# Performance work log

Hardware: AMD Instinct MI355X
Metric: run time of the kernel (lower is better)

## Reference

```python
import jax, jax.numpy as jnp
import numpy as np

N = 50000   # nodes
E = 800000  # edges (avg degree 16)
G = 64      # graphs in batch
DIMS = [96, 96, 96]  # gcn_layers_dim
RELU_LAYERS = [0, 1]


def setup_inputs() -> dict:
    key = jax.random.key(0)
    ks = jax.random.split(key, 32)
    inp = {
        "x": jax.random.normal(ks[0], (N, DIMS[0]), dtype=jnp.float32),
        "edge_index": jax.random.randint(ks[1], (2, E), 0, N, dtype=jnp.int64),
        "edge_weight": jax.random.uniform(ks[2], (E,), dtype=jnp.float32),
        "batch": jnp.sort(jax.random.randint(ks[3], (N,), 0, G, dtype=jnp.int64)),
        "edge_index_neighbor": jax.random.randint(ks[4], (2, E), 0, N, dtype=jnp.int64),
        "edge_weight_neighbor": jax.random.uniform(ks[5], (E,), dtype=jnp.float32),
        "batch_neighbor": jnp.sort(jax.random.randint(ks[6], (N,), 0, G, dtype=jnp.int64)),
    }
    ki = 7
    for l in range(len(DIMS) - 1):
        din, dout = DIMS[l], DIMS[l + 1]
        s = 1.0 / np.sqrt(din)
        inp[f"W{l}_o"] = jax.random.uniform(ks[ki + 0], (din, dout), minval=-s, maxval=s, dtype=jnp.float32)
        inp[f"b{l}_o"] = jnp.zeros((dout,), dtype=jnp.float32)
        inp[f"W{l}_n"] = jax.random.uniform(ks[ki + 1], (din, dout), minval=-s, maxval=s, dtype=jnp.float32)
        inp[f"b{l}_n"] = jnp.zeros((dout,), dtype=jnp.float32)
        sf = 1.0 / np.sqrt(2 * dout)
        inp[f"W{l}_f"] = jax.random.uniform(ks[ki + 2], (2 * dout, dout), minval=-sf, maxval=sf, dtype=jnp.float32)
        inp[f"b{l}_f"] = jax.random.uniform(ks[ki + 3], (dout,), minval=-sf, maxval=sf, dtype=jnp.float32)
        ki += 4
    return inp


def gcn_conv(x, W, b, edge_index, edge_weight, n):
    # PyG GCNConv: add self loops (weight 1), symmetric normalization, scatter-add.
    src, dst = edge_index[0], edge_index[1]
    deg = jax.ops.segment_sum(edge_weight, dst, num_segments=n) + 1.0  # +1 self loop
    dinv = jnp.where(deg > 0, jax.lax.rsqrt(deg), 0.0)  # [N]
    xw = x @ W  # [N, dout]
    norm = dinv[src] * edge_weight * dinv[dst]  # [E]
    out = jax.ops.segment_sum(norm[:, None] * xw[src], dst, num_segments=n)
    out = out + (dinv * dinv)[:, None] * xw  # self-loop contribution
    return out + b


def mean_pool(h, batch, g):
    s = jax.ops.segment_sum(h, batch, num_segments=g)
    c = jax.ops.segment_sum(jnp.ones((h.shape[0],), dtype=h.dtype), batch, num_segments=g)
    return s / jnp.maximum(c, 1.0)[:, None]


def reference(x, edge_index, edge_weight, batch, edge_index_neighbor,
              edge_weight_neighbor, batch_neighbor,
              W0_o, b0_o, W0_n, b0_n, W0_f, b0_f,
              W1_o, b1_o, W1_n, b1_n, W1_f, b1_f):
    params = [(W0_o, b0_o, W0_n, b0_n, W0_f, b0_f),
              (W1_o, b1_o, W1_n, b1_n, W1_f, b1_f)]
    n = x.shape[0]
    out = x
    embeddings = []
    for l, (Wo, bo, Wn, bn, Wf, bf) in enumerate(params):
        h_o = gcn_conv(out, Wo, bo, edge_index, edge_weight, n)
        h_n = gcn_conv(out, Wn, bn, edge_index_neighbor, edge_weight_neighbor, n)
        out = jnp.concatenate([h_o, h_n], axis=-1) @ Wf + bf
        if l in RELU_LAYERS:
            out = jax.nn.relu(out)
        embeddings.append(mean_pool(out, batch, G))
    return tuple(embeddings)
```

## Files before the change

### kernel.cpp

```cpp
#include <hip/hip_runtime.h>
#include <hip/hip_bf16.h>
#include <hip/hip_fp16.h>

#define DIM 96
#define EBLK 256
typedef unsigned int u32;
typedef unsigned long long u64;
typedef __attribute__((ext_vector_type(8))) _Float16 half8;
typedef __attribute__((ext_vector_type(4))) float f32x4;

__device__ __forceinline__ unsigned short f2h(float f) {
    union { unsigned short s; _Float16 h; } v; v.h = (_Float16)f; return v.s;
}
__device__ __forceinline__ u32 pkh(float lo, float hi) {
    return (u32)f2h(lo) | ((u32)f2h(hi) << 16);
}
__device__ __forceinline__ float hl(u32 u) {
    union { unsigned short s; _Float16 h; } v; v.s = (unsigned short)u; return (float)v.h;
}
__device__ __forceinline__ float hh(u32 u) {
    union { unsigned short s; _Float16 h; } v; v.s = (unsigned short)(u >> 16); return (float)v.h;
}

struct __align__(4) U3 { u32 a, b, c; };

__global__ __launch_bounds__(256) void k_cast0(
    const float* __restrict__ x, u32* __restrict__ Xh,
    const int* __restrict__ batch, int* __restrict__ gs, int* __restrict__ ge,
    float* __restrict__ outp, u32* __restrict__ cursor,
    int n, int total8, int osz)
{
    int i = blockIdx.x * 256 + threadIdx.x;
    if (i < total8) {
        const float4* xv = (const float4*)x;
        float4 a = xv[i * 2], b = xv[i * 2 + 1];
        uint4 o;
        o.x = pkh(a.x, a.y); o.y = pkh(a.z, a.w);
        o.z = pkh(b.x, b.y); o.w = pkh(b.z, b.w);
        ((uint4*)Xh)[i] = o;
    }
    if (i < n) {
        int b = batch[i];
        if (i == 0 || batch[i - 1] != b) gs[b] = i;
        if (i == n - 1 || batch[i + 1] != b) ge[b] = i + 1;
    }
    if (i < osz) outp[i] = 0.f;
    if (i == 0) { cursor[0] = 0; cursor[1] = 0; }
}

__global__ __launch_bounds__(256) void k_hist(
    const int* __restrict__ ei, const int* __restrict__ ein,
    u32* __restrict__ cntmat, int E, int n, int NB, int epb,
    const float* __restrict__ W0o, const float* __restrict__ W0n, const float* __restrict__ W0f,
    const float* __restrict__ b0o, const float* __restrict__ b0n, const float* __restrict__ b0f,
    const float* __restrict__ W1o, const float* __restrict__ W1n, const float* __restrict__ W1f,
    const float* __restrict__ b1o, const float* __restrict__ b1n, const float* __restrict__ b1f,
    unsigned short* __restrict__ Wt, float* __restrict__ bc,
    const int* __restrict__ gs, const int* __restrict__ ge, float* __restrict__ rinv)
{
    int set = blockIdx.y, tid = threadIdx.x;
    if (blockIdx.x >= EBLK) {
        if (blockIdx.y == 0 && blockIdx.x == EBLK && tid < 64) {
            int c = ge[tid] - gs[tid];
            if (c < 1) c = 1;
            rinv[tid] = 1.0f / (float)c;
        }
        int l = blockIdx.y;
        const float* Wo = l ? W1o : W0o;
        const float* Wn = l ? W1n : W0n;
        const float* Wf = l ? W1f : W0f;
        const float* bo = l ? b1o : b0o;
        const float* bn = l ? b1n : b0n;
        const float* bf = l ? b1f : b0f;
        unsigned short* wt = Wt + (size_t)l * 96 * 192;
        float* bcl = bc + l * DIM;
        int g = (blockIdx.x - EBLK) * 256 + tid;
        if (g >= DIM * DIM) return;
        int i = g / DIM, j = g % DIM;
        float so = 0.f, sn = 0.f;
        for (int k = 0; k < DIM; ++k) {
            so += Wo[i * DIM + k] * Wf[k * DIM + j];
            sn += Wn[i * DIM + k] * Wf[(DIM + k) * DIM + j];
        }
        wt[j * 192 + i]      = f2h(so);
        wt[j * 192 + 96 + i] = f2h(sn);
        if (i == 0) {
            float s = bf[j];
            for (int k = 0; k < DIM; ++k)
                s += bo[k] * Wf[k * DIM + j] + bn[k] * Wf[(DIM + k) * DIM + j];
            bcl[j] = s;
        }
        return;
    }
    __shared__ u32 hist[512];
    for (int t = tid; t < NB; t += 256) hist[t] = 0;
    __syncthreads();
    const int* D = (set ? ein : ei) + E;
    int lo = blockIdx.x * epb, hi = min(E, lo + epb);
    for (int e = lo + tid; e < hi; e += 256)
        atomicAdd(&hist[((u32)D[e]) >> 7], 1u);
    __syncthreads();
    u32* cm = cntmat + (size_t)set * NB * EBLK;
    for (int t = tid; t < NB; t += 256)
        cm[(size_t)t * EBLK + blockIdx.x] = hist[t];
}

__global__ __launch_bounds__(256) void k_bscan(
    const u32* __restrict__ cntmat, u32* __restrict__ ebase,
    u64* __restrict__ binfo, u32* __restrict__ cursor, int NB)
{
    int set = blockIdx.y, b = blockIdx.x, tid = threadIdx.x;
    int lane = tid & 63, wv = tid >> 6;
    const u32* cm = cntmat + ((size_t)set * NB + b) * EBLK;
    u32 v = cm[tid];
    u32 incl = v;
    #pragma unroll
    for (int d = 1; d < 64; d <<= 1) {
        u32 t = __shfl_up(incl, d);
        if (lane >= d) incl += t;
    }
    __shared__ u32 wt[4], woff[4], base_s;
    if (lane == 63) wt[wv] = incl;
    __syncthreads();
    if (tid == 0) {
        u32 run = 0;
        #pragma unroll
        for (int k = 0; k < 4; ++k) { woff[k] = run; run += wt[k]; }
        base_s = atomicAdd(&cursor[set], run);
        binfo[(size_t)set * NB + b] = ((u64)run << 32) | (u64)base_s;
    }
    __syncthreads();
    ebase[((size_t)set * NB + b) * EBLK + tid] = base_s + woff[wv] + incl - v;
}

__global__ __launch_bounds__(256) void k_part(
    const int* __restrict__ ei, const float* __restrict__ ew,
    const int* __restrict__ ein, const float* __restrict__ ewn,
    const u32* __restrict__ ebase, u64* __restrict__ evb,
    int E, int NB, int epb)
{
    int set = blockIdx.y, tid = threadIdx.x;
    const int*   I = set ? ein : ei;
    const float* W = set ? ewn : ew;
    __shared__ u32 hb[512];
    const u32* eb = ebase + (size_t)set * NB * EBLK;
    for (int t = tid; t < NB; t += 256) hb[t] = eb[(size_t)t * EBLK + blockIdx.x];
    __syncthreads();
    u64* out = evb + (size_t)set * E;
    int lo = blockIdx.x * epb, hi = min(E, lo + epb);
    for (int e = lo + tid; e < hi; e += 256) {
        int s = I[e], d = I[E + e];
        u32 wbits = __float_as_uint(W[e]);
        u32 pos = atomicAdd(&hb[(u32)d >> 7], 1u);
        out[pos] = ((u64)wbits << 32) | ((u32)(d & 127) << 17) | (u32)s;
    }
}

__global__ __launch_bounds__(256) void k_nprep(
    const u64* __restrict__ evb, const u64* __restrict__ binfo,
    u64* __restrict__ seg, float* __restrict__ dinv, int E, int n, int NB)
{
    int set = blockIdx.y, b = blockIdx.x, tid = threadIdx.x;
    __shared__ u64 acc[128];
    if (tid < 128) acc[tid] = 0;
    __syncthreads();
    u64 bi = binfo[(size_t)set * NB + b];
    u32 base = (u32)bi, tot = (u32)(bi >> 32);
    const u64* ev = evb + (size_t)set * E;
    for (u32 j = tid; j < tot; j += 256) {
        u64 p = ev[base + j];
        u32 dl = ((u32)p >> 17) & 127;
        float w = __uint_as_float((u32)(p >> 32));
        u32 wfix = (u32)(w * 16777216.0f + 0.5f);
        atomicAdd(&acc[dl], ((u64)1 << 32) | (u64)wfix);
    }
    __syncthreads();
    __shared__ u32 wtot;
    u32 cnt = 0, excl = 0;
    if (tid < 128) {
        u64 a = acc[tid];
        cnt = (u32)(a >> 32);
        u32 incl = cnt;
        #pragma unroll
        for (int d = 1; d < 64; d <<= 1) {
            u32 t = __shfl_up(incl, d);
            if ((tid & 63) >= d) incl += t;
        }
        if (tid == 63) wtot = incl;
        excl = incl - cnt;
    }
    __syncthreads();
    if (tid >= 64 && tid < 128) excl += wtot;
    int gnode = b * 128 + tid;
    if (tid < 128 && gnode < n) {
        u32 st = base + excl;
        seg[(size_t)set * n + gnode] = ((u64)(st + cnt) << 32) | (u64)st;
        u64 a = acc[tid];
        dinv[(size_t)set * n + gnode] =
            rsqrtf((float)(u32)a * 5.9604644775390625e-8f + 1.0f);
    }
}

__global__ __launch_bounds__(256) void k_scat2(
    const u64* __restrict__ evb, const u64* __restrict__ binfo,
    const u64* __restrict__ seg, const float* __restrict__ dinv,
    u64* __restrict__ evout, int E, int n, int NB)
{
    int set = blockIdx.y, b = blockIdx.x, tid = threadIdx.x;
    __shared__ u32 rk[128];
    __shared__ u32 st_l[128];
    __shared__ float dv_l[128];
    const float* dv = dinv + (size_t)set * n;
    if (tid < 128) {
        rk[tid] = 0;
        int gnode = b * 128 + tid;
        if (gnode < n) {
            st_l[tid] = (u32)seg[(size_t)set * n + gnode];
            dv_l[tid] = dv[gnode];
        }
    }
    __syncthreads();
    u64 bi = binfo[(size_t)set * NB + b];
    u32 base = (u32)bi, tot = (u32)(bi >> 32);
    const u64* evi = evb + (size_t)set * E;
    u64* out = evout + (size_t)set * E;
    for (u32 j = tid; j < tot; j += 256) {
        u64 p = evi[base + j];
        u32 src = (u32)p & 0x1ffffu;
        u32 dl = ((u32)p >> 17) & 127;
        float w = __uint_as_float((u32)(p >> 32));
        float nrm = dv_l[dl] * w * dv[src];
        u32 slot = st_l[dl] + atomicAdd(&rk[dl], 1u);
        out[slot] = ((u64)__float_as_uint(nrm) << 32) | (u64)src;
    }
}

__global__ __launch_bounds__(256) void k_agg(
    const u32* __restrict__ Xh,
    const u64* __restrict__ seg,
    const u64* __restrict__ ev_o, const u64* __restrict__ ev_n,
    const float* __restrict__ dinv,
    u32* __restrict__ fAB, int n)
{
    int wid = (blockIdx.x * 256 + threadIdx.x) >> 6;
    if (wid >= n) return;
    int lane = threadIdx.x & 63;
    int g = lane >> 4, sl = lane & 15;
    const u64* ev; const u64* sg; const float* dv; int co;
    if (blockIdx.y) { sg = seg + n; ev = ev_n; dv = dinv + n; co = 48; }
    else            { sg = seg;     ev = ev_o; dv = dinv;     co = 0; }

    float a0=0,a1=0,a2=0,a3=0,a4=0,a5=0;
    if (g == 0) {
        float dr = dv[wid];
        float d2 = dr * dr;
        U3 xv = *(const U3*)(Xh + (size_t)wid * 48 + sl * 3);
        a0 = d2 * hl(xv.a); a1 = d2 * hh(xv.a);
        a2 = d2 * hl(xv.b); a3 = d2 * hh(xv.b);
        a4 = d2 * hl(xv.c); a5 = d2 * hh(xv.c);
    }
    u64 sv = sg[wid];
    int s = (int)(u32)sv, e = (int)(u32)(sv >> 32);
    if (e > s) {
        int j0 = s + g;
        float ww[8]; int uu[8];
        #pragma unroll
        for (int k = 0; k < 8; ++k) {
            int j = j0 + k * 4;
            int jc = j < e ? j : s;
            u64 t = ev[jc];
            ww[k] = (j < e) ? __uint_as_float((u32)(t >> 32)) : 0.f;
            uu[k] = (int)(u32)t;
        }
        U3 xx[8];
        #pragma unroll
        for (int k = 0; k < 8; ++k)
            xx[k] = *(const U3*)(Xh + (size_t)uu[k] * 48 + sl * 3);
        #pragma unroll
        for (int k = 0; k < 8; ++k) {
            float w = ww[k];
            a0 += w * hl(xx[k].a); a1 += w * hh(xx[k].a);
            a2 += w * hl(xx[k].b); a3 += w * hh(xx[k].b);
            a4 += w * hl(xx[k].c); a5 += w * hh(xx[k].c);
        }
        for (int j = j0 + 32; j < e; j += 4) {
            u64 ee = ev[j];
            int u = (int)(u32)ee;
            float w = __uint_as_float((u32)(ee >> 32));
            U3 xv = *(const U3*)(Xh + (size_t)u * 48 + sl * 3);
            a0 += w * hl(xv.a); a1 += w * hh(xv.a);
            a2 += w * hl(xv.b); a3 += w * hh(xv.b);
            a4 += w * hl(xv.c); a5 += w * hh(xv.c);
        }
    }
    a0 += __shfl_xor(a0, 32); a1 += __shfl_xor(a1, 32); a2 += __shfl_xor(a2, 32);
    a3 += __shfl_xor(a3, 32); a4 += __shfl_xor(a4, 32); a5 += __shfl_xor(a5, 32);
    a0 += __shfl_xor(a0, 16); a1 += __shfl_xor(a1, 16); a2 += __shfl_xor(a2, 16);
    a3 += __shfl_xor(a3, 16); a4 += __shfl_xor(a4, 16); a5 += __shfl_xor(a5, 16);
    if (g == 0) {
        U3 o;
        o.a = pkh(a0, a1); o.b = pkh(a2, a3); o.c = pkh(a4, a5);
        *(U3*)(fAB + (size_t)wid * 96 + co + sl * 3) = o;
    }
}

__global__ __launch_bounds__(256) void k_mmp(
    const u32* __restrict__ fAB, const unsigned short* __restrict__ Wtg,
    const float* __restrict__ bias, const int* __restrict__ batch,
    const int* __restrict__ gs, const int* __restrict__ ge,
    const float* __restrict__ rinv, float* __restrict__ outp,
    u32* __restrict__ Hh, int writeH, int n)
{
    __shared__ unsigned short sW[96 * 200];
    __shared__ float tile[64][100];
    int tid = threadIdx.x;
    for (int m = tid; m < 2304; m += 256) {
        int j = m / 24, k = (m % 24) * 8;
        *(uint4*)&sW[j * 200 + k] = *(const uint4*)&Wtg[j * 192 + k];
    }
    __syncthreads();
    int r0 = blockIdx.x * 64;
    int rows = min(64, n - r0);
    int lane = tid & 63, wv = tid >> 6;
    int rl = lane & 15;
    int kg = lane >> 4;
    int rowg = r0 + wv * 16 + rl;
    int rc = min(rowg, n - 1);
    const half8* Arow = (const half8*)(fAB + (size_t)rc * 96);
    f32x4 acc[6];
    #pragma unroll
    for (int c = 0; c < 6; ++c) acc[c] = (f32x4){0.f, 0.f, 0.f, 0.f};
    #pragma unroll
    for (int t = 0; t < 6; ++t) {
        half8 a = Arow[t * 4 + kg];
        #pragma unroll
        for (int c = 0; c < 6; ++c) {
            half8 b = *(const half8*)&sW[(c * 16 + rl) * 200 + t * 32 + kg * 8];
            acc[c] = __builtin_amdgcn_mfma_f32_16x16x32_f16(a, b, acc[c], 0, 0, 0);
        }
    }
    #pragma unroll
    for (int c = 0; c < 6; ++c) {
        int col = c * 16 + rl;
        float bs = bias[col];
        #pragma unroll
        for (int q = 0; q < 4; ++q) {
            int lr = wv * 16 + kg * 4 + q;
            tile[lr][col] = fmaxf(acc[c][q] + bs, 0.f);
        }
    }
    __syncthreads();
    if (writeH) {
        for (int m = tid; m < rows * 48; m += 256) {
            int row = m / 48, cp = m % 48;
            Hh[(size_t)(r0 + row) * 48 + cp] = pkh(tile[row][cp * 2], tile[row][cp * 2 + 1]);
        }
    }
    if (tid < DIM) {
        int gfirst = batch[r0], glast = batch[r0 + rows - 1];
        for (int g = gfirst; g <= glast; ++g) {
            int lo = max(gs[g] - r0, 0), hi = min(ge[g] - r0, rows);
            if (lo < hi) {
                float s = 0.f;
                for (int r = lo; r < hi; ++r) s += tile[r][tid];
                atomicAdd(&outp[g * DIM + tid], s * rinv[g]);
            }
        }
    }
}

extern "C" void kernel_launch(void* const* d_in, const int* in_sizes, int n_in,
                              void* d_out, int out_size, void* d_ws, size_t ws_size,
                              hipStream_t stream)
{
    const float* x     = (const float*)d_in[0];
    const int*   ei    = (const int*)d_in[1];
    const float* ew    = (const float*)d_in[2];
    const int*   batch = (const int*)d_in[3];
    const int*   ein   = (const int*)d_in[4];
    const float* ewn   = (const float*)d_in[5];
    const float* W0o = (const float*)d_in[7];
    const float* b0o = (const float*)d_in[8];
    const float* W0n = (const float*)d_in[9];
    const float* b0n = (const float*)d_in[10];
    const float* W0f = (const float*)d_in[11];
    const float* b0f = (const float*)d_in[12];
    const float* W1o = (const float*)d_in[13];
    const float* b1o = (const float*)d_in[14];
    const float* W1n = (const float*)d_in[15];
    const float* b1n = (const float*)d_in[16];
    const float* W1f = (const float*)d_in[17];
    const float* b1f = (const float*)d_in[18];

    const int N = in_sizes[0] / DIM;
    const int E = in_sizes[2];
    float* out = (float*)d_out;
    const int NB = (N + 127) >> 7;
    const int epb = (E + EBLK - 1) / EBLK;

    char* ws = (char*)d_ws;
    size_t off = 0;
    auto alloc = [&](size_t bytes) -> char* {
        char* p = ws + off;
        off += (bytes + 255) & ~(size_t)255;
        return p;
    };
    u32*   cntmat = (u32*)alloc((size_t)2 * NB * EBLK * 4);
    u32*   ebase  = (u32*)alloc((size_t)2 * NB * EBLK * 4);
    u64*   binfo  = (u64*)alloc((size_t)2 * NB * 8);
    u64*   evb    = (u64*)alloc((size_t)2 * E * 8);
    u64*   ev     = (u64*)alloc((size_t)2 * E * 8);
    u64*   seg    = (u64*)alloc((size_t)2 * N * 8);
    float* dinv   = (float*)alloc((size_t)2 * N * 4);
    u32*   Xh     = (u32*)alloc((size_t)N * 48 * 4);
    u32*   Hh     = (u32*)alloc((size_t)N * 48 * 4);
    u32*   fAB    = (u32*)alloc((size_t)N * 96 * 4);
    unsigned short* Wt = (unsigned short*)alloc((size_t)2 * 96 * 192 * 2);
    float* bc     = (float*)alloc(2 * DIM * 4);
    float* rinv   = (float*)alloc(64 * 4);
    int*   gs     = (int*)alloc(64 * 4);
    int*   ge     = (int*)alloc(64 * 4);
    u32*   cursor = (u32*)alloc(2 * 4);

    k_cast0<<<(N * 12 + 255) / 256, 256, 0, stream>>>(x, Xh, batch, gs, ge, out, cursor,
                                                      N, N * 12, out_size);
    k_hist<<<dim3(EBLK + 36, 2), 256, 0, stream>>>(ei, ein, cntmat, E, N, NB, epb,
                                                   W0o, W0n, W0f, b0o, b0n, b0f,
                                                   W1o, W1n, W1f, b1o, b1n, b1f,
                                                   Wt, bc, gs, ge, rinv);
    k_bscan<<<dim3(NB, 2), 256, 0, stream>>>(cntmat, ebase, binfo, cursor, NB);
    k_part<<<dim3(EBLK, 2), 256, 0, stream>>>(ei, ew, ein, ewn, ebase, evb, E, NB, epb);
    k_nprep<<<dim3(NB, 2), 256, 0, stream>>>(evb, binfo, seg, dinv, E, N, NB);
    k_scat2<<<dim3(NB, 2), 256, 0, stream>>>(evb, binfo, seg, dinv, ev, E, N, NB);

    dim3 ag(((size_t)N * 64 + 255) / 256, 2);
    int mb = (N + 63) / 64;

    k_agg<<<ag, 256, 0, stream>>>(Xh, seg, ev, ev + E, dinv, fAB, N);
    k_mmp<<<mb, 256, 0, stream>>>(fAB, Wt, bc, batch, gs, ge, rinv, out, Hh, 1, N);
    k_agg<<<ag, 256, 0, stream>>>(Hh, seg, ev, ev + E, dinv, fAB, N);
    k_mmp<<<mb, 256, 0, stream>>>(fAB, Wt + (size_t)96 * 192, bc + DIM, batch, gs, ge, rinv,
                                  out + 64 * DIM, Hh, 0, N);
}
```

Baseline: 220.5 us.

## Map one 16-lane group per node in aggregation instead of one wavefront

The aggregation kernel now gives each node a 16-lane group, so one wavefront handles four nodes instead of one. Each group walks the node's edge list serially in unrolled chunks of 8 and writes its own result. This removes the cross-group shuffle reduction and cuts the grid size by four. The cost is more serial edge iterations per group and possible divergence across groups with unequal degrees.

```diff
diff --git a/kernel.cpp b/kernel.cpp
--- a/kernel.cpp
+++ b/kernel.cpp
@@ -242,35 +242,33 @@
     const float* __restrict__ dinv,
     u32* __restrict__ fAB, int n)
 {
-    int wid = (blockIdx.x * 256 + threadIdx.x) >> 6;
-    if (wid >= n) return;
+    int gw = (blockIdx.x * 256 + threadIdx.x) >> 6;
     int lane = threadIdx.x & 63;
     int g = lane >> 4, sl = lane & 15;
+    int node = gw * 4 + g;
+    if (node >= n) return;
     const u64* ev; const u64* sg; const float* dv; int co;
     if (blockIdx.y) { sg = seg + n; ev = ev_n; dv = dinv + n; co = 48; }
     else            { sg = seg;     ev = ev_o; dv = dinv;     co = 0; }
 
-    float a0=0,a1=0,a2=0,a3=0,a4=0,a5=0;
-    if (g == 0) {
-        float dr = dv[wid];
-        float d2 = dr * dr;
-        U3 xv = *(const U3*)(Xh + (size_t)wid * 48 + sl * 3);
-        a0 = d2 * hl(xv.a); a1 = d2 * hh(xv.a);
-        a2 = d2 * hl(xv.b); a3 = d2 * hh(xv.b);
-        a4 = d2 * hl(xv.c); a5 = d2 * hh(xv.c);
-    }
-    u64 sv = sg[wid];
+    float dr = dv[node];
+    float d2 = dr * dr;
+    U3 xs = *(const U3*)(Xh + (size_t)node * 48 + sl * 3);
+    float a0 = d2 * hl(xs.a), a1 = d2 * hh(xs.a);
+    float a2 = d2 * hl(xs.b), a3 = d2 * hh(xs.b);
+    float a4 = d2 * hl(xs.c), a5 = d2 * hh(xs.c);
+
+    u64 sv = sg[node];
     int s = (int)(u32)sv, e = (int)(u32)(sv >> 32);
-    if (e > s) {
-        int j0 = s + g;
+    for (int j = s; j < e; j += 8) {
         float ww[8]; int uu[8];
         #pragma unroll
         for (int k = 0; k < 8; ++k) {
-            int j = j0 + k * 4;
-            int jc = j < e ? j : s;
-            u64 t = ev[jc];
-            ww[k] = (j < e) ? __uint_as_float((u32)(t >> 32)) : 0.f;
-            uu[k] = (int)(u32)t;
+            int jj = j + k;
+            bool v = jj < e;
+            u64 t = ev[v ? jj : j];
+            ww[k] = v ? __uint_as_float((u32)(t >> 32)) : 0.f;
+            uu[k] = v ? (int)(u32)t : node;
         }
         U3 xx[8];
         #pragma unroll
@@ -283,25 +281,10 @@
             a2 += w * hl(xx[k].b); a3 += w * hh(xx[k].b);
             a4 += w * hl(xx[k].c); a5 += w * hh(xx[k].c);
         }
-        for (int j = j0 + 32; j < e; j += 4) {
-            u64 ee = ev[j];
-            int u = (int)(u32)ee;
-            float w = __uint_as_float((u32)(ee >> 32));
-            U3 xv = *(const U3*)(Xh + (size_t)u * 48 + sl * 3);
-            a0 += w * hl(xv.a); a1 += w * hh(xv.a);
-            a2 += w * hl(xv.b); a3 += w * hh(xv.b);
-            a4 += w * hl(xv.c); a5 += w * hh(xv.c);
-        }
-    }
-    a0 += __shfl_xor(a0, 32); a1 += __shfl_xor(a1, 32); a2 += __shfl_xor(a2, 32);
-    a3 += __shfl_xor(a3, 32); a4 += __shfl_xor(a4, 32); a5 += __shfl_xor(a5, 32);
-    a0 += __shfl_xor(a0, 16); a1 += __shfl_xor(a1, 16); a2 += __shfl_xor(a2, 16);
-    a3 += __shfl_xor(a3, 16); a4 += __shfl_xor(a4, 16); a5 += __shfl_xor(a5, 16);
-    if (g == 0) {
-        U3 o;
-        o.a = pkh(a0, a1); o.b = pkh(a2, a3); o.c = pkh(a4, a5);
-        *(U3*)(fAB + (size_t)wid * 96 + co + sl * 3) = o;
-    }
+    }
+    U3 o;
+    o.a = pkh(a0, a1); o.b = pkh(a2, a3); o.c = pkh(a4, a5);
+    *(U3*)(fAB + (size_t)node * 96 + co + sl * 3) = o;
 }
 
 __global__ __launch_bounds__(256) void k_mmp(
@@ -433,7 +416,7 @@
     k_nprep<<<dim3(NB, 2), 256, 0, stream>>>(evb, binfo, seg, dinv, E, N, NB);
     k_scat2<<<dim3(NB, 2), 256, 0, stream>>>(evb, binfo, seg, dinv, ev, E, N, NB);
 
-    dim3 ag(((size_t)N * 64 + 255) / 256, 2);
+    dim3 ag((N + 15) / 16, 2);
     int mb = (N + 63) / 64;
 
     k_agg<<<ag, 256, 0, stream>>>(Xh, seg, ev, ev + E, dinv, fAB, N);
```

Result: faster. 198.1 us (-10.2%).
